# Kernel optimization log

Measured on AMD Instinct MI355X. Metric: run time of the kernel, lower is better.

Reference implementation:

```python
import jax, jax.numpy as jnp
import numpy as np
import math

CHUNK = 256
NUM_HEADS = 4
EPS = 1e-5


def setup_inputs() -> dict:
    key = jax.random.key(0)
    ks = jax.random.split(key, 12)
    B, N, F = 4, 2048, 256
    x = jax.random.normal(ks[0], (B, N, F), dtype=jnp.float32)
    adj_matrix = jax.random.randint(ks[1], (N, N), 0, 2, dtype=jnp.int32)
    s = 1.0 / math.sqrt(F)
    Wq = jax.random.normal(ks[2], (F, F), dtype=jnp.float32) * s
    bq = jnp.zeros((F,), dtype=jnp.float32)
    Wk = jax.random.normal(ks[3], (F, F), dtype=jnp.float32) * s
    bk = jnp.zeros((F,), dtype=jnp.float32)
    Wv = jax.random.normal(ks[4], (F, F), dtype=jnp.float32) * s
    bv = jnp.zeros((F,), dtype=jnp.float32)
    Wo = jax.random.normal(ks[5], (F, F), dtype=jnp.float32) * s
    bo = jnp.zeros((F,), dtype=jnp.float32)
    gamma = jnp.ones((F,), dtype=jnp.float32)
    beta = jnp.zeros((F,), dtype=jnp.float32)
    return {"x": x, "adj_matrix": adj_matrix, "Wq": Wq, "bq": bq, "Wk": Wk,
            "bk": bk, "Wv": Wv, "bv": bv, "Wo": Wo, "bo": bo,
            "gamma": gamma, "beta": beta}


def reference(x, adj_matrix, Wq, bq, Wk, bk, Wv, bv, Wo, bo, gamma, beta):
    B, N, Fin = x.shape
    H = NUM_HEADS
    Dout = Wq.shape[0]
    Dh = Dout // H
    Nc = N // CHUNK  # number of key chunks

    # projections -> [B, H, N, Dh]
    q = (x @ Wq.T + bq).reshape(B, N, H, Dh).transpose(0, 2, 1, 3)
    k = (x @ Wk.T + bk).reshape(B, N, H, Dh).transpose(0, 2, 1, 3)
    v = (x @ Wv.T + bv).reshape(B, N, H, Dh).transpose(0, 2, 1, 3)

    # key/value chunks: [B, H, Nc, CHUNK, Dh]
    kc = k.reshape(B, H, Nc, CHUNK, Dh)
    vc = v.reshape(B, H, Nc, CHUNK, Dh)

    # scores per key chunk: [B, H, N, Nc, CHUNK]
    scores = jnp.einsum('bhnd,bhjcd->bhnjc', q, kc) / jnp.sqrt(
        jnp.asarray(Dh, dtype=q.dtype))
    scores = jnp.clip(scores, -10.0, 10.0)
    # adjacency mask, chunked along keys: [1, 1, N, Nc, CHUNK]
    mask = adj_matrix.reshape(N, Nc, CHUNK)[None, None]
    scores = jnp.where(mask == 0, jnp.asarray(-10.0, scores.dtype), scores)

    # FAITHFUL quirk: softmax is taken per key chunk (last axis only) and the
    # per-chunk contexts are SUMMED -> total attention mass per query is Nc.
    attn = jax.nn.softmax(scores, axis=-1)
    ctx = jnp.einsum('bhnjc,bhjcd->bhnd', attn, vc)  # sum over chunks j

    ctx = ctx.transpose(0, 2, 1, 3).reshape(B, N, Dout)
    out = ctx @ Wo.T + bo
    out = out + x  # residual (in_features == out_features)

    mu = jnp.mean(out, axis=-1, keepdims=True)
    var = jnp.mean(jnp.square(out - mu), axis=-1, keepdims=True)
    out = (out - mu) * jax.lax.rsqrt(var + EPS) * gamma + beta
    return out
```

## Files before the change

### kernel.cpp

```cpp
#include <hip/hip_runtime.h>
#include <math.h>

#define B_     4
#define N_     2048
#define F_     256
#define H_     4
#define DH     64
#define BN     8192
#define SP     72
#define SPO    136
#define SPW    264

#define QSCALE 0.18033688011112042f
#define CLIP   14.426950408889634f

typedef _Float16 f16;
typedef _Float16 half8  __attribute__((ext_vector_type(8)));
typedef _Float16 half4v __attribute__((ext_vector_type(4)));
typedef float    floatx4 __attribute__((ext_vector_type(4)));
typedef unsigned long long u64;

__global__ __launch_bounds__(256) void prep_kernel(
    const int* __restrict__ adj, u64* __restrict__ P,
    const float* __restrict__ x,  f16* __restrict__ xh,
    const float* __restrict__ Wq, f16* __restrict__ Wqh,
    const float* __restrict__ Wk, f16* __restrict__ Wkh,
    const float* __restrict__ Wv, f16* __restrict__ Wvh,
    const float* __restrict__ Wo, f16* __restrict__ Woh)
{
    const int bid = blockIdx.x;
    if (bid < 16384) {
        const int row   = bid >> 3;
        const int chunk = bid & 7;
        const int wave  = threadIdx.x >> 6, lane = threadIdx.x & 63;
        const int key   = chunk * 256 + wave * 64 + lane;
        u64 m = __ballot(adj[(size_t)row * N_ + key] != 0);
        if (lane == 0) P[(size_t)row * 32 + chunk * 4 + wave] = m;
        return;
    }
    const float* src; f16* dst; int base;
    if      (bid < 16448) { src = Wo; dst = Woh; base = (bid - 16384) * 1024; }
    else if (bid < 16512) { src = Wq; dst = Wqh; base = (bid - 16448) * 1024; }
    else if (bid < 16576) { src = Wk; dst = Wkh; base = (bid - 16512) * 1024; }
    else if (bid < 16640) { src = Wv; dst = Wvh; base = (bid - 16576) * 1024; }
    else                  { src = x;  dst = xh;  base = (bid - 16640) * 1024; }
    const int idx = base + threadIdx.x * 4;
    float4 v = *(const float4*)(src + idx);
    half4v h; h[0] = (f16)v.x; h[1] = (f16)v.y; h[2] = (f16)v.z; h[3] = (f16)v.w;
    *(half4v*)(dst + idx) = h;
}

__global__ __launch_bounds__(256) void proj_mfma(
    const f16* __restrict__ xh,
    const f16* __restrict__ Wqh, const f16* __restrict__ Wkh, const f16* __restrict__ Wvh,
    const float* __restrict__ bq, const float* __restrict__ bk, const float* __restrict__ bv,
    f16* __restrict__ Qh, f16* __restrict__ Kh, f16* __restrict__ Vt)
{
    const int which = blockIdx.z;
    const f16*   W    = which == 0 ? Wqh : which == 1 ? Wkh : Wvh;
    const float* bias = which == 0 ? bq  : which == 1 ? bk  : bv;

    const int r0 = blockIdx.x * 64;
    const int c0 = blockIdx.y * 128;
    const int tid  = threadIdx.x;
    const int wave = tid >> 6, lane = tid & 63;
    const int quad = lane >> 4, l16 = lane & 15;
    const int row  = tid >> 2, seg  = tid & 3;
    const int wrow = tid >> 1, whalf = (tid & 1) * 32;

    __shared__ f16 smem[(64 + 128) * SP];
    f16* xs = smem;
    f16* wt = smem + 64 * SP;

    floatx4 zz = {0.f, 0.f, 0.f, 0.f};
    floatx4 acc[8] = {zz, zz, zz, zz, zz, zz, zz, zz};

    for (int f0 = 0; f0 < F_; f0 += 64) {
        const f16* xsrc = xh + (size_t)(r0 + row) * F_ + f0 + seg * 16;
        const f16* wsrc = W  + (size_t)(c0 + wrow) * F_ + f0 + whalf;
        float4 xa0 = *(const float4*)(xsrc),      xa1 = *(const float4*)(xsrc + 8);
        float4 wa0 = *(const float4*)(wsrc),      wa1 = *(const float4*)(wsrc + 8);
        float4 wa2 = *(const float4*)(wsrc + 16), wa3 = *(const float4*)(wsrc + 24);
        __syncthreads();
        *(float4*)&xs[row * SP + seg * 16]      = xa0;
        *(float4*)&xs[row * SP + seg * 16 + 8]  = xa1;
        *(float4*)&wt[wrow * SP + whalf]        = wa0;
        *(float4*)&wt[wrow * SP + whalf + 8]    = wa1;
        *(float4*)&wt[wrow * SP + whalf + 16]   = wa2;
        *(float4*)&wt[wrow * SP + whalf + 24]   = wa3;
        __syncthreads();
        half8 a0 = *(const half8*)&xs[(wave * 16 + l16) * SP + quad * 8];
        half8 a1 = *(const half8*)&xs[(wave * 16 + l16) * SP + 32 + quad * 8];
#pragma unroll
        for (int ot = 0; ot < 8; ot++) {
            half8 b0 = *(const half8*)&wt[(ot * 16 + l16) * SP + quad * 8];
            half8 b1 = *(const half8*)&wt[(ot * 16 + l16) * SP + 32 + quad * 8];
            acc[ot] = __builtin_amdgcn_mfma_f32_16x16x32_f16(a0, b0, acc[ot], 0, 0, 0);
            acc[ot] = __builtin_amdgcn_mfma_f32_16x16x32_f16(a1, b1, acc[ot], 0, 0, 0);
        }
    }

    const int bb = r0 >> 11, nn0 = r0 & (N_ - 1);

    if (which == 2) {
#pragma unroll
        for (int ot = 0; ot < 8; ot++) {
            const int o  = c0 + ot * 16 + l16;
            const int hy = o >> 6, dh = o & 63;
            const float bv_ = bias[o];
            half4v h4;
#pragma unroll
            for (int r = 0; r < 4; r++) h4[r] = (f16)(acc[ot][r] + bv_);
            *(half4v*)(Vt + (((size_t)bb * H_ + hy) * DH + dh) * N_
                          + nn0 + wave * 16 + quad * 4) = h4;
        }
    } else {
        const float scl = (which == 0) ? QSCALE : 1.0f;
        f16* dst = which == 0 ? Qh : Kh;
        __syncthreads();
        f16* outb = smem;
#pragma unroll
        for (int ot = 0; ot < 8; ot++) {
            const float bv_ = bias[c0 + ot * 16 + l16];
#pragma unroll
            for (int r = 0; r < 4; r++)
                outb[(wave * 16 + quad * 4 + r) * SPO + ot * 16 + l16] =
                    (f16)((acc[ot][r] + bv_) * scl);
        }
        __syncthreads();
        const int colb = seg * 32;
        const int hh = (c0 + colb) >> 6, dcol = (c0 + colb) & 63;
        f16* g = dst + (((size_t)bb * H_ + hh) * N_ + nn0 + row) * DH + dcol;
#pragma unroll
        for (int k = 0; k < 4; k++)
            *(float4*)(g + k * 8) = *(const float4*)&outb[row * SPO + colb + k * 8];
    }
}

__global__ __launch_bounds__(512) void attn_mfma(
    const f16* __restrict__ Qh, const f16* __restrict__ Kh,
    const f16* __restrict__ Vt, const u64* __restrict__ Padj,
    f16* __restrict__ CTXP)
{
    const int nt = blockIdx.x & 15;
    const int sp = blockIdx.x >> 4;
    const int qb = nt * 128;
    const int h  = blockIdx.y;
    const int b  = blockIdx.z;
    const int bh = b * H_ + h;
    const int tid  = threadIdx.x;
    const int wave = tid >> 6, lane = tid & 63;
    const int quad = lane >> 4, l16 = lane & 15;
    const int qrow = tid >> 2, qseg = tid & 3;
    const int kvr  = tid >> 3, kvs  = tid & 7;

    __shared__ f16 QPs[128 * SP];
    __shared__ f16 Ks[64 * SP];
    __shared__ f16 Vs[64 * SP];

    {
        const f16* src = Qh + ((size_t)bh * N_ + qb + qrow) * DH + qseg * 16;
        *(float4*)&QPs[qrow * SP + qseg * 16]     = *(const float4*)(src);
        *(float4*)&QPs[qrow * SP + qseg * 16 + 8] = *(const float4*)(src + 8);
    }
    __syncthreads();
    const half8 qf0 = *(const half8*)&QPs[(wave * 16 + l16) * SP + quad * 8];
    const half8 qf1 = *(const half8*)&QPs[(wave * 16 + l16) * SP + 32 + quad * 8];
    f16* Ps = QPs + wave * 16 * SP;

    const int qglob = qb + wave * 16 + l16;
    const u64* arow = Padj + (size_t)qglob * 32;

    floatx4 zz = {0.f, 0.f, 0.f, 0.f};
    floatx4 ctx_tot[4] = {zz, zz, zz, zz};

    for (int ci = 0; ci < 2; ci++) {
        const int c = sp * 2 + ci;
        floatx4 ctx_ch[4] = {zz, zz, zz, zz};
        float rs_ch = 0.f;

        for (int kt = 0; kt < 4; kt++) {
            const int k0 = c * 256 + kt * 64;
            const f16* ksrc = Kh + ((size_t)bh * N_ + k0 + kvr) * DH + kvs * 8;
            const f16* vsrc = Vt + ((size_t)bh * DH + kvr) * N_ + k0 + kvs * 8;
            float4 ka = *(const float4*)(ksrc);
            float4 va = *(const float4*)(vsrc);
            __syncthreads();
            *(float4*)&Ks[kvr * SP + kvs * 8] = ka;
            *(float4*)&Vs[kvr * SP + kvs * 8] = va;
            __syncthreads();

            const u64 aw = arow[k0 >> 6];
            float rs = 0.f;
#pragma unroll
            for (int m = 0; m < 4; m++) {
                floatx4 sacc = zz;
                half8 a0 = *(const half8*)&Ks[(m * 16 + l16) * SP + quad * 8];
                half8 a1 = *(const half8*)&Ks[(m * 16 + l16) * SP + 32 + quad * 8];
                sacc = __builtin_amdgcn_mfma_f32_16x16x32_f16(a0, qf0, sacc, 0, 0, 0);
                sacc = __builtin_amdgcn_mfma_f32_16x16x32_f16(a1, qf1, sacc, 0, 0, 0);
                const unsigned int nib = (unsigned int)(aw >> (m * 16 + quad * 4)) & 0xFu;
                half4v pv;
#pragma unroll
                for (int r = 0; r < 4; r++) {
                    float sv = fminf(fmaxf(sacc[r], -CLIP), CLIP);
                    sv = ((nib >> r) & 1u) ? sv : -CLIP;
                    const float ev = __builtin_amdgcn_exp2f(sv);
                    rs += ev;
                    pv[r] = (f16)ev;
                }
                *(half4v*)&Ps[l16 * SP + m * 16 + quad * 4] = pv;
            }
            rs += __shfl_xor(rs, 16);
            rs += __shfl_xor(rs, 32);
            rs_ch += rs;

            const half8 p0 = *(const half8*)&Ps[l16 * SP + quad * 8];
            const half8 p1 = *(const half8*)&Ps[l16 * SP + 32 + quad * 8];
#pragma unroll
            for (int m = 0; m < 4; m++) {
                half8 va8 = *(const half8*)&Vs[(m * 16 + l16) * SP + quad * 8];
                half8 vb8 = *(const half8*)&Vs[(m * 16 + l16) * SP + 32 + quad * 8];
                ctx_ch[m] = __builtin_amdgcn_mfma_f32_16x16x32_f16(va8, p0, ctx_ch[m], 0, 0, 0);
                ctx_ch[m] = __builtin_amdgcn_mfma_f32_16x16x32_f16(vb8, p1, ctx_ch[m], 0, 0, 0);
            }
        }

        const float inv = 1.0f / rs_ch;
#pragma unroll
        for (int m = 0; m < 4; m++)
#pragma unroll
            for (int r = 0; r < 4; r++)
                ctx_tot[m][r] += ctx_ch[m][r] * inv;
    }

    f16* dst = CTXP + (((size_t)sp * B_ + b) * N_ + qglob) * F_ + h * DH;
#pragma unroll
    for (int m = 0; m < 4; m++) {
        half4v h4;
#pragma unroll
        for (int r = 0; r < 4; r++) h4[r] = (f16)ctx_tot[m][r];
        *(half4v*)&dst[m * 16 + quad * 4] = h4;
    }
}

__global__ __launch_bounds__(256) void out_mfma(
    const f16* __restrict__ CTXP, const float* __restrict__ x,
    const f16* __restrict__ Woh, const float* __restrict__ bo,
    const float* __restrict__ gamma, const float* __restrict__ beta,
    float* __restrict__ out)
{
    const int n0 = blockIdx.x * 32;
    const int tid  = threadIdx.x;
    const int wave = tid >> 6, lane = tid & 63;
    const int quad = lane >> 4, l16 = lane & 15;
    const int wrow = tid >> 2, wseg = tid & 3;

    __shared__ f16 cs[32 * SPW];
    __shared__ f16 wtile[256 * SP];
    __shared__ float red0[4][32], red1[4][32];

    {
        const int row = tid >> 4, c0 = (tid & 15) * 16;
        const size_t S = (size_t)BN * F_;
#pragma unroll
        for (int g2 = 0; g2 < 2; g2++) {
            const int rr = g2 * 16 + row;
            const f16* p = CTXP + (size_t)(n0 + rr) * F_ + c0;
#pragma unroll
            for (int g = 0; g < 2; g++) {
                half8 s0 = *(const half8*)(p + g * 8);
                half8 s1 = *(const half8*)(p + S + g * 8);
                half8 s2 = *(const half8*)(p + 2 * S + g * 8);
                half8 s3 = *(const half8*)(p + 3 * S + g * 8);
                half8 o;
#pragma unroll
                for (int e = 0; e < 8; e++)
                    o[e] = (f16)(((float)s0[e] + (float)s1[e]) + ((float)s2[e] + (float)s3[e]));
                *(half8*)&cs[rr * SPW + c0 + g * 8] = o;
            }
        }
    }

    floatx4 zz = {0.f, 0.f, 0.f, 0.f};
    floatx4 acc[2][4] = {{zz, zz, zz, zz}, {zz, zz, zz, zz}};

#pragma unroll
    for (int f0 = 0; f0 < F_; f0 += 64) {
        __syncthreads();
#pragma unroll
        for (int rr = 0; rr < 4; rr++) {
            const int o = rr * 64 + wrow;
            const f16* src = Woh + (size_t)o * F_ + f0 + wseg * 16;
            *(float4*)&wtile[o * SP + wseg * 16]     = *(const float4*)(src);
            *(float4*)&wtile[o * SP + wseg * 16 + 8] = *(const float4*)(src + 8);
        }
        __syncthreads();
        half8 a00 = *(const half8*)&cs[l16 * SPW + f0 + quad * 8];
        half8 a01 = *(const half8*)&cs[l16 * SPW + f0 + 32 + quad * 8];
        half8 a10 = *(const half8*)&cs[(16 + l16) * SPW + f0 + quad * 8];
        half8 a11 = *(const half8*)&cs[(16 + l16) * SPW + f0 + 32 + quad * 8];
#pragma unroll
        for (int ot = 0; ot < 4; ot++) {
            const int o = wave * 64 + ot * 16 + l16;
            half8 b0 = *(const half8*)&wtile[o * SP + quad * 8];
            half8 b1 = *(const half8*)&wtile[o * SP + 32 + quad * 8];
            acc[0][ot] = __builtin_amdgcn_mfma_f32_16x16x32_f16(a00, b0, acc[0][ot], 0, 0, 0);
            acc[0][ot] = __builtin_amdgcn_mfma_f32_16x16x32_f16(a01, b1, acc[0][ot], 0, 0, 0);
            acc[1][ot] = __builtin_amdgcn_mfma_f32_16x16x32_f16(a10, b0, acc[1][ot], 0, 0, 0);
            acc[1][ot] = __builtin_amdgcn_mfma_f32_16x16x32_f16(a11, b1, acc[1][ot], 0, 0, 0);
        }
    }

#pragma unroll
    for (int g2 = 0; g2 < 2; g2++)
#pragma unroll
        for (int ot = 0; ot < 4; ot++) {
            const int o = wave * 64 + ot * 16 + l16;
            const float bo_ = bo[o];
#pragma unroll
            for (int r = 0; r < 4; r++)
                acc[g2][ot][r] += bo_ + x[(size_t)(n0 + g2 * 16 + quad * 4 + r) * F_ + o];
        }

#pragma unroll
    for (int g2 = 0; g2 < 2; g2++)
#pragma unroll
        for (int r = 0; r < 4; r++) {
            float s = (acc[g2][0][r] + acc[g2][1][r]) + (acc[g2][2][r] + acc[g2][3][r]);
            float q = (acc[g2][0][r] * acc[g2][0][r] + acc[g2][1][r] * acc[g2][1][r]) +
                      (acc[g2][2][r] * acc[g2][2][r] + acc[g2][3][r] * acc[g2][3][r]);
            s += __shfl_xor(s, 1); q += __shfl_xor(q, 1);
            s += __shfl_xor(s, 2); q += __shfl_xor(q, 2);
            s += __shfl_xor(s, 4); q += __shfl_xor(q, 4);
            s += __shfl_xor(s, 8); q += __shfl_xor(q, 8);
            if (l16 == 0) {
                red0[wave][g2 * 16 + quad * 4 + r] = s;
                red1[wave][g2 * 16 + quad * 4 + r] = q;
            }
        }
    __syncthreads();

#pragma unroll
    for (int g2 = 0; g2 < 2; g2++)
#pragma unroll
        for (int r = 0; r < 4; r++) {
            const int rr = g2 * 16 + quad * 4 + r;
            const float S  = (red0[0][rr] + red0[1][rr]) + (red0[2][rr] + red0[3][rr]);
            const float Q2 = (red1[0][rr] + red1[1][rr]) + (red1[2][rr] + red1[3][rr]);
            const float mu  = S * (1.0f / F_);
            const float var = Q2 * (1.0f / F_) - mu * mu;
            const float inv = rsqrtf(var + 1e-5f);
#pragma unroll
            for (int ot = 0; ot < 4; ot++) {
                const int o = wave * 64 + ot * 16 + l16;
                out[(size_t)(n0 + rr) * F_ + o] =
                    (acc[g2][ot][r] - mu) * inv * gamma[o] + beta[o];
            }
        }
}

extern "C" void kernel_launch(void* const* d_in, const int* in_sizes, int n_in,
                              void* d_out, int out_size, void* d_ws, size_t ws_size,
                              hipStream_t stream)
{
    const float* x     = (const float*)d_in[0];
    const int*   adj   = (const int*)  d_in[1];
    const float* Wq    = (const float*)d_in[2];
    const float* bq    = (const float*)d_in[3];
    const float* Wk    = (const float*)d_in[4];
    const float* bk    = (const float*)d_in[5];
    const float* Wv    = (const float*)d_in[6];
    const float* bv    = (const float*)d_in[7];
    const float* Wo    = (const float*)d_in[8];
    const float* bo    = (const float*)d_in[9];
    const float* gamma = (const float*)d_in[10];
    const float* beta  = (const float*)d_in[11];
    float* out = (float*)d_out;

    float* ws = (float*)d_ws;
    f16*   CTXP = (f16*)(ws);
    f16*   Qh   = (f16*)(ws + 4194304);
    f16*   Kh   = (f16*)(ws + 5242880);
    f16*   Vt   = (f16*)(ws + 6291456);
    u64*   Padj = (u64*)(ws + 7340032);
    f16*   Woh  = (f16*)(ws + 7471104);
    f16*   xh   = CTXP;
    f16*   Wqh  = (f16*)(ws + 1048576);
    f16*   Wkh  = (f16*)(ws + 1081344);
    f16*   Wvh  = (f16*)(ws + 1114112);

    hipLaunchKernelGGL(prep_kernel, dim3(18688), dim3(256), 0, stream,
                       adj, Padj, x, xh, Wq, Wqh, Wk, Wkh, Wv, Wvh, Wo, Woh);
    hipLaunchKernelGGL(proj_mfma, dim3(BN / 64, 2, 3), dim3(256), 0, stream,
                       xh, Wqh, Wkh, Wvh, bq, bk, bv, Qh, Kh, Vt);
    hipLaunchKernelGGL(attn_mfma, dim3(64, H_, B_), dim3(512), 0, stream,
                       Qh, Kh, Vt, Padj, CTXP);
    hipLaunchKernelGGL(out_mfma, dim3(BN / 32), dim3(256), 0, stream,
                       CTXP, x, Woh, bo, gamma, beta, out);
}
```

Before: 156.3 us.

## Use 32x32 MFMA tiles in attention and split work per key chunk

The attention kernel moves from 16x16x32 MFMA tiles to 32x32x16 tiles. Each wave now handles 32 queries with 256-thread blocks, and each block processes a single 256-key chunk instead of two, so the grid doubles and the context writes eight partial slices. The output kernel sums eight partial context buffers instead of four, and the workspace layout is enlarged to hold them. This aims to cut LDS traffic per MFMA and raise parallelism, at the cost of twice the partial-context memory traffic in the reduction step.

Result: no change. 154.7 us (-1.0%).

```diff
diff --git a/kernel.cpp b/kernel.cpp
--- a/kernel.cpp
+++ b/kernel.cpp
@@ -17,7 +17,8 @@
 typedef _Float16 f16;
 typedef _Float16 half8  __attribute__((ext_vector_type(8)));
 typedef _Float16 half4v __attribute__((ext_vector_type(4)));
-typedef float    floatx4 __attribute__((ext_vector_type(4)));
+typedef float    floatx4  __attribute__((ext_vector_type(4)));
+typedef float    floatx16 __attribute__((ext_vector_type(16)));
 typedef unsigned long long u64;
 
 __global__ __launch_bounds__(256) void prep_kernel(
@@ -137,7 +138,7 @@
     }
 }
 
-__global__ __launch_bounds__(512) void attn_mfma(
+__global__ __launch_bounds__(256) void attn_mfma(
     const f16* __restrict__ Qh, const f16* __restrict__ Kh,
     const f16* __restrict__ Vt, const u64* __restrict__ Padj,
     f16* __restrict__ CTXP)
@@ -150,97 +151,101 @@
     const int bh = b * H_ + h;
     const int tid  = threadIdx.x;
     const int wave = tid >> 6, lane = tid & 63;
-    const int quad = lane >> 4, l16 = lane & 15;
-    const int qrow = tid >> 2, qseg = tid & 3;
-    const int kvr  = tid >> 3, kvs  = tid & 7;
+    const int l31 = lane & 31, hf = lane >> 5;
 
     __shared__ f16 QPs[128 * SP];
     __shared__ f16 Ks[64 * SP];
     __shared__ f16 Vs[64 * SP];
 
     {
-        const f16* src = Qh + ((size_t)bh * N_ + qb + qrow) * DH + qseg * 16;
-        *(float4*)&QPs[qrow * SP + qseg * 16]     = *(const float4*)(src);
-        *(float4*)&QPs[qrow * SP + qseg * 16 + 8] = *(const float4*)(src + 8);
+        const int qrow = tid >> 1, qhalf = (tid & 1) * 32;
+        const f16* src = Qh + ((size_t)bh * N_ + qb + qrow) * DH + qhalf;
+#pragma unroll
+        for (int k = 0; k < 4; k++)
+            *(float4*)&QPs[qrow * SP + qhalf + k * 8] = *(const float4*)(src + k * 8);
     }
     __syncthreads();
-    const half8 qf0 = *(const half8*)&QPs[(wave * 16 + l16) * SP + quad * 8];
-    const half8 qf1 = *(const half8*)&QPs[(wave * 16 + l16) * SP + 32 + quad * 8];
-    f16* Ps = QPs + wave * 16 * SP;
-
-    const int qglob = qb + wave * 16 + l16;
+    half8 qf[4];
+#pragma unroll
+    for (int s = 0; s < 4; s++)
+        qf[s] = *(const half8*)&QPs[(wave * 32 + l31) * SP + s * 16 + hf * 8];
+    f16* Ps = QPs + wave * 32 * SP;
+
+    const int qglob = qb + wave * 32 + l31;
     const u64* arow = Padj + (size_t)qglob * 32;
 
-    floatx4 zz = {0.f, 0.f, 0.f, 0.f};
-    floatx4 ctx_tot[4] = {zz, zz, zz, zz};
-
-    for (int ci = 0; ci < 2; ci++) {
-        const int c = sp * 2 + ci;
-        floatx4 ctx_ch[4] = {zz, zz, zz, zz};
-        float rs_ch = 0.f;
-
-        for (int kt = 0; kt < 4; kt++) {
-            const int k0 = c * 256 + kt * 64;
-            const f16* ksrc = Kh + ((size_t)bh * N_ + k0 + kvr) * DH + kvs * 8;
-            const f16* vsrc = Vt + ((size_t)bh * DH + kvr) * N_ + k0 + kvs * 8;
-            float4 ka = *(const float4*)(ksrc);
-            float4 va = *(const float4*)(vsrc);
-            __syncthreads();
-            *(float4*)&Ks[kvr * SP + kvs * 8] = ka;
-            *(float4*)&Vs[kvr * SP + kvs * 8] = va;
-            __syncthreads();
-
-            const u64 aw = arow[k0 >> 6];
-            float rs = 0.f;
-#pragma unroll
-            for (int m = 0; m < 4; m++) {
-                floatx4 sacc = zz;
-                half8 a0 = *(const half8*)&Ks[(m * 16 + l16) * SP + quad * 8];
-                half8 a1 = *(const half8*)&Ks[(m * 16 + l16) * SP + 32 + quad * 8];
-                sacc = __builtin_amdgcn_mfma_f32_16x16x32_f16(a0, qf0, sacc, 0, 0, 0);
-                sacc = __builtin_amdgcn_mfma_f32_16x16x32_f16(a1, qf1, sacc, 0, 0, 0);
-                const unsigned int nib = (unsigned int)(aw >> (m * 16 + quad * 4)) & 0xFu;
+    floatx16 ctx0 = {0.f,0.f,0.f,0.f,0.f,0.f,0.f,0.f,0.f,0.f,0.f,0.f,0.f,0.f,0.f,0.f};
+    floatx16 ctx1 = ctx0;
+    const floatx16 z16 = ctx0;
+    float rs_ch = 0.f;
+
+    const int kvr = tid >> 2, kvs = (tid & 3) * 16;
+
+    for (int kt = 0; kt < 4; kt++) {
+        const int k0 = sp * 256 + kt * 64;
+        const f16* ksrc = Kh + ((size_t)bh * N_ + k0 + kvr) * DH + kvs;
+        const f16* vsrc = Vt + ((size_t)bh * DH + kvr) * N_ + k0 + kvs;
+        float4 ka0 = *(const float4*)(ksrc), ka1 = *(const float4*)(ksrc + 8);
+        float4 va0 = *(const float4*)(vsrc), va1 = *(const float4*)(vsrc + 8);
+        __syncthreads();
+        *(float4*)&Ks[kvr * SP + kvs]     = ka0;
+        *(float4*)&Ks[kvr * SP + kvs + 8] = ka1;
+        *(float4*)&Vs[kvr * SP + kvs]     = va0;
+        *(float4*)&Vs[kvr * SP + kvs + 8] = va1;
+        __syncthreads();
+
+        const u64 aw = arow[k0 >> 6];
+        float rs = 0.f;
+
+#pragma unroll
+        for (int m = 0; m < 2; m++) {
+            floatx16 sacc = z16;
+#pragma unroll
+            for (int s = 0; s < 4; s++) {
+                half8 a = *(const half8*)&Ks[(m * 32 + l31) * SP + s * 16 + hf * 8];
+                sacc = __builtin_amdgcn_mfma_f32_32x32x16_f16(a, qf[s], sacc, 0, 0, 0);
+            }
+#pragma unroll
+            for (int rg = 0; rg < 4; rg++) {
+                const unsigned int nib =
+                    (unsigned int)(aw >> (m * 32 + rg * 8 + hf * 4)) & 0xFu;
                 half4v pv;
 #pragma unroll
                 for (int r = 0; r < 4; r++) {
-                    float sv = fminf(fmaxf(sacc[r], -CLIP), CLIP);
+                    float sv = fminf(fmaxf(sacc[rg * 4 + r], -CLIP), CLIP);
                     sv = ((nib >> r) & 1u) ? sv : -CLIP;
                     const float ev = __builtin_amdgcn_exp2f(sv);
                     rs += ev;
                     pv[r] = (f16)ev;
                 }
-                *(half4v*)&Ps[l16 * SP + m * 16 + quad * 4] = pv;
+                *(half4v*)&Ps[l31 * SP + m * 32 + rg * 8 + hf * 4] = pv;
             }
-            rs += __shfl_xor(rs, 16);
-            rs += __shfl_xor(rs, 32);
-            rs_ch += rs;
-
-            const half8 p0 = *(const half8*)&Ps[l16 * SP + quad * 8];
-            const half8 p1 = *(const half8*)&Ps[l16 * SP + 32 + quad * 8];
-#pragma unroll
-            for (int m = 0; m < 4; m++) {
-                half8 va8 = *(const half8*)&Vs[(m * 16 + l16) * SP + quad * 8];
-                half8 vb8 = *(const half8*)&Vs[(m * 16 + l16) * SP + 32 + quad * 8];
-                ctx_ch[m] = __builtin_amdgcn_mfma_f32_16x16x32_f16(va8, p0, ctx_ch[m], 0, 0, 0);
-                ctx_ch[m] = __builtin_amdgcn_mfma_f32_16x16x32_f16(vb8, p1, ctx_ch[m], 0, 0, 0);
-            }
-        }
-
-        const float inv = 1.0f / rs_ch;
-#pragma unroll
-        for (int m = 0; m < 4; m++)
-#pragma unroll
-            for (int r = 0; r < 4; r++)
-                ctx_tot[m][r] += ctx_ch[m][r] * inv;
-    }
-
+        }
+        rs += __shfl_xor(rs, 32);
+        rs_ch += rs;
+
+#pragma unroll
+        for (int s = 0; s < 4; s++) {
+            half8 pf = *(const half8*)&Ps[l31 * SP + s * 16 + hf * 8];
+            half8 v0 = *(const half8*)&Vs[l31 * SP + s * 16 + hf * 8];
+            half8 v1 = *(const half8*)&Vs[(32 + l31) * SP + s * 16 + hf * 8];
+            ctx0 = __builtin_amdgcn_mfma_f32_32x32x16_f16(v0, pf, ctx0, 0, 0, 0);
+            ctx1 = __builtin_amdgcn_mfma_f32_32x32x16_f16(v1, pf, ctx1, 0, 0, 0);
+        }
+    }
+
+    const float inv = 1.0f / rs_ch;
     f16* dst = CTXP + (((size_t)sp * B_ + b) * N_ + qglob) * F_ + h * DH;
 #pragma unroll
-    for (int m = 0; m < 4; m++) {
-        half4v h4;
-#pragma unroll
-        for (int r = 0; r < 4; r++) h4[r] = (f16)ctx_tot[m][r];
-        *(half4v*)&dst[m * 16 + quad * 4] = h4;
+    for (int rg = 0; rg < 4; rg++) {
+        half4v h0, h1;
+#pragma unroll
+        for (int r = 0; r < 4; r++) {
+            h0[r] = (f16)(ctx0[rg * 4 + r] * inv);
+            h1[r] = (f16)(ctx1[rg * 4 + r] * inv);
+        }
+        *(half4v*)&dst[rg * 8 + hf * 4]      = h0;
+        *(half4v*)&dst[32 + rg * 8 + hf * 4] = h1;
     }
 }
 
@@ -269,14 +274,16 @@
             const f16* p = CTXP + (size_t)(n0 + rr) * F_ + c0;
 #pragma unroll
             for (int g = 0; g < 2; g++) {
-                half8 s0 = *(const half8*)(p + g * 8);
-                half8 s1 = *(const half8*)(p + S + g * 8);
-                half8 s2 = *(const half8*)(p + 2 * S + g * 8);
-                half8 s3 = *(const half8*)(p + 3 * S + g * 8);
+                float v[8] = {0.f,0.f,0.f,0.f,0.f,0.f,0.f,0.f};
+#pragma unroll
+                for (int pp = 0; pp < 8; pp++) {
+                    half8 s = *(const half8*)(p + (size_t)pp * S + g * 8);
+#pragma unroll
+                    for (int e = 0; e < 8; e++) v[e] += (float)s[e];
+                }
                 half8 o;
 #pragma unroll
-                for (int e = 0; e < 8; e++)
-                    o[e] = (f16)(((float)s0[e] + (float)s1[e]) + ((float)s2[e] + (float)s3[e]));
+                for (int e = 0; e < 8; e++) o[e] = (f16)v[e];
                 *(half8*)&cs[rr * SPW + c0 + g * 8] = o;
             }
         }
@@ -380,11 +387,11 @@
 
     float* ws = (float*)d_ws;
     f16*   CTXP = (f16*)(ws);
-    f16*   Qh   = (f16*)(ws + 4194304);
-    f16*   Kh   = (f16*)(ws + 5242880);
-    f16*   Vt   = (f16*)(ws + 6291456);
-    u64*   Padj = (u64*)(ws + 7340032);
-    f16*   Woh  = (f16*)(ws + 7471104);
+    f16*   Qh   = (f16*)(ws + 8388608);
+    f16*   Kh   = (f16*)(ws + 9437184);
+    f16*   Vt   = (f16*)(ws + 10485760);
+    u64*   Padj = (u64*)(ws + 11534336);
+    f16*   Woh  = (f16*)(ws + 11665408);
     f16*   xh   = CTXP;
     f16*   Wqh  = (f16*)(ws + 1048576);
     f16*   Wkh  = (f16*)(ws + 1081344);
@@ -394,7 +401,7 @@
                        adj, Padj, x, xh, Wq, Wqh, Wk, Wkh, Wv, Wvh, Wo, Woh);
     hipLaunchKernelGGL(proj_mfma, dim3(BN / 64, 2, 3), dim3(256), 0, stream,
                        xh, Wqh, Wkh, Wvh, bq, bk, bv, Qh, Kh, Vt);
-    hipLaunchKernelGGL(attn_mfma, dim3(64, H_, B_), dim3(512), 0, stream,
+    hipLaunchKernelGGL(attn_mfma, dim3(128, H_, B_), dim3(256), 0, stream,
                        Qh, Kh, Vt, Padj, CTXP);
     hipLaunchKernelGGL(out_mfma, dim3(BN / 32), dim3(256), 0, stream,
                        CTXP, x, Woh, bo, gamma, beta, out);
```
